# Optimization experiments

Measured on AMD Instinct MI355X. Metric: run time of the kernel, lower is better.

Reference implementation:

```python
import jax, jax.numpy as jnp
import numpy as np

N, E, IN, H, HEADS, L, OUT = 4096, 262144, 64, 128, 4, 2, 2
DH = H // HEADS  # 32, per-head dim for both GAT and global MHA
BN_EPS = 1e-5
NEG_SLOPE = 0.2  # GATConv leaky_relu default


def setup_inputs() -> dict:
    key = jax.random.key(0)
    ks = iter(jax.random.split(key, 32))
    rn = lambda shape, s: jax.random.normal(next(ks), shape, jnp.float32) * s
    return {
        "x": rn((N, IN), 1.0),
        "edge_index": jax.random.randint(next(ks), (2, E), 0, N),
        "w_in": rn((H, IN), IN ** -0.5),
        "b_in": rn((H,), 0.02),
        "w_gat": rn((L, H, H), H ** -0.5),
        "att_src": rn((L, HEADS, DH), 0.1),
        "att_dst": rn((L, HEADS, DH), 0.1),
        "b_gat": rn((L, H), 0.02),
        "w_qkv": rn((L, 3 * H, H), H ** -0.5),
        "b_qkv": rn((L, 3 * H), 0.02),
        "w_o": rn((L, H, H), H ** -0.5),
        "b_o": rn((L, H), 0.02),
        "bn_gamma": 1.0 + rn((L, 3, H), 0.05),
        "bn_beta": rn((L, 3, H), 0.05),
        "w1": rn((L, 2 * H, H), H ** -0.5),
        "b1": rn((L, 2 * H), 0.02),
        "w2": rn((L, H, 2 * H), (2 * H) ** -0.5),
        "b2": rn((L, H), 0.02),
        "w_out": rn((OUT, H), H ** -0.5),
        "b_out": rn((OUT,), 0.02),
    }


def _bn(h, g, b):
    # eval-mode BatchNorm1d with running_mean=0, running_var=1
    return h * (g / jnp.sqrt(1.0 + BN_EPS)) + b


def _gat(x, src, dst, w, a_src, a_dst, bias):
    # GATConv(hidden, hidden//heads, heads=HEADS, add_self_loops=False), concat=True
    xp = (x @ w.T).reshape(N, HEADS, DH)                  # [N, HEADS, DH]
    al_s = jnp.einsum('nhd,hd->nh', xp, a_src)            # [N, HEADS]
    al_d = jnp.einsum('nhd,hd->nh', xp, a_dst)
    logit = al_s[src] + al_d[dst]                         # [E, HEADS]
    logit = jnp.where(logit >= 0, logit, NEG_SLOPE * logit)
    m = jax.ops.segment_max(logit, dst, num_segments=N)   # scatter-softmax over dst
    m = jnp.where(jnp.isfinite(m), m, 0.0)
    e = jnp.exp(logit - m[dst])
    denom = jax.ops.segment_sum(e, dst, num_segments=N)
    alpha = e / (denom[dst] + 1e-16)
    out = jax.ops.segment_sum(alpha[:, :, None] * xp[src], dst, num_segments=N)
    return out.reshape(N, H) + bias


def _mha(x, wqkv, bqkv, wo, bo):
    # torch.nn.MultiheadAttention self-attention over all N nodes (one graph)
    qkv = x @ wqkv.T + bqkv
    q, k, v = jnp.split(qkv, 3, axis=-1)
    q = q.reshape(N, HEADS, DH)
    k = k.reshape(N, HEADS, DH)
    v = v.reshape(N, HEADS, DH)
    scores = jnp.einsum('nhd,mhd->hnm', q, k) / jnp.sqrt(jnp.float32(DH))
    attn = jax.nn.softmax(scores, axis=-1)
    out = jnp.einsum('hnm,mhd->nhd', attn, v).reshape(N, H)
    return out @ wo.T + bo


def reference(x, edge_index, w_in, b_in, w_gat, att_src, att_dst, b_gat,
              w_qkv, b_qkv, w_o, b_o, bn_gamma, bn_beta,
              w1, b1, w2, b2, w_out, b_out):
    src, dst = edge_index[0], edge_index[1]
    h = jax.nn.relu(x @ w_in.T + b_in)
    for l in range(L):
        # GPSConv: local GAT branch (dropout inactive in eval)
        h_loc = _gat(h, src, dst, w_gat[l], att_src[l], att_dst[l], b_gat[l]) + h
        h_loc = _bn(h_loc, bn_gamma[l, 0], bn_beta[l, 0])
        # GPSConv: global attention branch
        h_att = _mha(h, w_qkv[l], b_qkv[l], w_o[l], b_o[l]) + h
        h_att = _bn(h_att, bn_gamma[l, 1], bn_beta[l, 1])
        out = h_loc + h_att
        mlp = jax.nn.relu(out @ w1[l].T + b1[l]) @ w2[l].T + b2[l]
        out = _bn(out + mlp, bn_gamma[l, 2], bn_beta[l, 2])
        # GPSRiskModel residual + relu (dropout inactive in eval)
        h = jax.nn.relu(out + h)
    return h @ w_out.T + b_out
```

## Files before the change

kernel.cpp:

```cpp
#include <hip/hip_runtime.h>

#define NN 4096
#define EE 262144
#define INF_ 64
#define HH 128
#define HEADS 4
#define DH 32
#define LL 2
#define NH (NN * HH)
#define KSPLIT 16
#define L2E 1.4426950408889634f

typedef unsigned short u16;
typedef unsigned int u32;
using bf16x8 = __attribute__((ext_vector_type(8))) short;
using f32x4 = __attribute__((ext_vector_type(4))) float;

__device__ __forceinline__ float bf2f(u16 v) { return __uint_as_float(((u32)v) << 16); }
__device__ __forceinline__ u16 f2bf(float f) {
    u32 u = __float_as_uint(f);
    u32 r = (u + 0x7fffu + ((u >> 16) & 1u)) >> 16;
    return (u16)r;
}
__device__ __forceinline__ u32 encf(float f) {
    u32 b = __float_as_uint(f);
    return (b & 0x80000000u) ? ~b : (b | 0x80000000u);
}
__device__ __forceinline__ float decf(u32 u) {
    u32 b = (u & 0x80000000u) ? (u & 0x7fffffffu) : ~u;
    return __uint_as_float(b);
}

__global__ __launch_bounds__(256) void k_detect(const u16* __restrict__ x, int* __restrict__ flag,
                                                int* __restrict__ cnt, u32* __restrict__ gmax) {
    int t = threadIdx.x;
    for (int i = t; i < NN; i += 256) cnt[i] = 0;
    if (t < 16) gmax[t] = 0;
    __shared__ int cs[256];
    u16 v = x[2 * t];
    int e = (v >> 7) & 0xFF;
    cs[t] = (e >= 100 && e <= 140) ? 1 : 0;
    __syncthreads();
    for (int s = 128; s > 0; s >>= 1) {
        if (t < s) cs[t] += cs[t + s];
        __syncthreads();
    }
    if (t == 0) *flag = (cs[0] >= 128) ? 1 : 0;
}

#define MAXSEG 16
struct SegF { const void* src[MAXSEG]; int dst[MAXSEG]; int n[MAXSEG]; int cnt; };
struct SegB { const void* src[8]; u16* dst[8]; u16* dst2[8]; int n[8]; int cnt; };
__global__ __launch_bounds__(256) void k_prep(SegF SF, float* __restrict__ W, SegB SB,
                                              const int* __restrict__ flag,
                                              const int* __restrict__ dst, int* __restrict__ cnt) {
    int bid = blockIdx.x, t = threadIdx.x;
    if (bid < 96) {
        int seg = bid >> 3, bx = bid & 7;
        if (seg >= SF.cnt) return;
        int n = SF.n[seg];
        float* d = W + SF.dst[seg];
        const void* s = SF.src[seg];
        int f = *flag;
        for (int i = bx * 256 + t; i < n; i += 8 * 256)
            d[i] = f ? bf2f(((const u16*)s)[i]) : ((const float*)s)[i];
    } else if (bid < 992) {
        int b2 = bid - 96;
        int seg = b2 >> 7, bx = b2 & 127;
        if (seg >= SB.cnt) return;
        int f = *flag;
        u16* d = SB.dst[seg];
        u16* d2 = SB.dst2[seg];
        if (f && !d2) return;
        int n = SB.n[seg];
        const void* s = SB.src[seg];
        for (int i = bx * 256 + t; i < n; i += 128 * 256) {
            if (d2) {
                float v = f ? bf2f(((const u16*)s)[i]) : ((const float*)s)[i];
                u16 h = f2bf(v);
                d[i] = h;
                d2[i] = f2bf(v - bf2f(h));
            } else {
                d[i] = f2bf(((const float*)s)[i]);
            }
        }
    } else {
        int e = (bid - 992) * 256 + t;
        if (e < EE) atomicAdd(&cnt[dst[e]], 1);
    }
}

__global__ __launch_bounds__(128) void k_mgemm(const u16* __restrict__ Ahi, const u16* __restrict__ Alo,
                                               const u16* __restrict__ Wc, const u16* __restrict__ Wd,
                                               const int* __restrict__ flag,
                                               const float* __restrict__ bias,
                                               float* __restrict__ outf, u16* __restrict__ outb16,
                                               u16* __restrict__ outhi, u16* __restrict__ outlo,
                                               int K, int J, int relu, int jtiles,
                                               const int* __restrict__ scnt, int* __restrict__ srowstart,
                                               int* __restrict__ scursor) {
    __shared__ int part[128];
    if ((int)blockIdx.y >= jtiles) {
        if (blockIdx.x != 0 || scnt == nullptr) return;
        int t = threadIdx.x;
        int loc[32];
        int s = 0;
#pragma unroll
        for (int i = 0; i < 32; ++i) { loc[i] = s; s += scnt[t * 32 + i]; }
        part[t] = s;
        __syncthreads();
        for (int off = 1; off < 128; off <<= 1) {
            int v = part[t];
            int a = (t >= off) ? part[t - off] : 0;
            __syncthreads();
            part[t] = v + a;
            __syncthreads();
        }
        int base = (t == 0) ? 0 : part[t - 1];
#pragma unroll
        for (int i = 0; i < 32; ++i) {
            srowstart[t * 32 + i] = base + loc[i];
            scursor[t * 32 + i] = base + loc[i];
        }
        return;
    }
    const u16* Wb = (*flag) ? Wd : Wc;
    int wave = threadIdx.x >> 6, lane = threadIdx.x & 63;
    int grp = lane >> 4, lcol = lane & 15;
    int m0 = blockIdx.x * 32 + wave * 16;
    int j0 = blockIdx.y * 64;
    f32x4 acc[4];
#pragma unroll
    for (int s = 0; s < 4; ++s) acc[s] = (f32x4){0.f, 0.f, 0.f, 0.f};
    const u16* ah = Ahi + (size_t)(m0 + lcol) * K + grp * 8;
    const u16* al = Alo + (size_t)(m0 + lcol) * K + grp * 8;
    const u16* wb = Wb + (size_t)(j0 + lcol) * K + grp * 8;
    for (int k = 0; k < K; k += 32) {
        bf16x8 va = *(const bf16x8*)(ah + k);
        bf16x8 vl = *(const bf16x8*)(al + k);
#pragma unroll
        for (int s = 0; s < 4; ++s) {
            bf16x8 vw = *(const bf16x8*)(wb + (size_t)s * 16 * K + k);
            acc[s] = __builtin_amdgcn_mfma_f32_16x16x32_bf16(va, vw, acc[s], 0, 0, 0);
            acc[s] = __builtin_amdgcn_mfma_f32_16x16x32_bf16(vl, vw, acc[s], 0, 0, 0);
        }
    }
#pragma unroll
    for (int s = 0; s < 4; ++s) {
        int col = j0 + s * 16 + lcol;
        float bs = bias ? bias[col] : 0.f;
#pragma unroll
        for (int r = 0; r < 4; ++r) {
            float v = acc[s][r] + bs;
            if (relu) v = fmaxf(v, 0.f);
            size_t idx = (size_t)(m0 + grp * 4 + r) * J + col;
            if (outf) outf[idx] = v;
            if (outb16) outb16[idx] = f2bf(v);
            if (outhi) {
                u16 hv = f2bf(v);
                outhi[idx] = hv;
                outlo[idx] = f2bf(v - bf2f(hv));
            }
        }
    }
}

__global__ __launch_bounds__(128) void k_gemm_gq(const u16* __restrict__ Ahi, const u16* __restrict__ Alo,
                                                 const u16* __restrict__ wgatc, const u16* __restrict__ wgatd,
                                                 const u16* __restrict__ wqkvc, const u16* __restrict__ wqkvd,
                                                 const int* __restrict__ flag,
                                                 const float* __restrict__ bqkv,
                                                 u16* __restrict__ xpb, u16* __restrict__ qkvb,
                                                 const int* __restrict__ esrc_src, const int* __restrict__ esrc_dst,
                                                 int* __restrict__ cursor, int* __restrict__ esrc) {
    if (blockIdx.y >= 8) {
        int b = (blockIdx.y - 8) * 128 + blockIdx.x;
        for (int e = b * 128 + threadIdx.x; e < EE; e += 32768) {
            int d = esrc_dst[e];
            int p = atomicAdd(&cursor[d], 1);
            esrc[p] = esrc_src[e];
        }
        return;
    }
    int wave = threadIdx.x >> 6, lane = threadIdx.x & 63;
    int grp = lane >> 4, lcol = lane & 15;
    int m0 = blockIdx.x * 32 + wave * 16;
    int jb = blockIdx.y;
    int j0 = jb * 64;
    int f = *flag;
    const u16* wgat = f ? wgatd : wgatc;
    const u16* wqkv = f ? wqkvd : wqkvc;
    const u16* Wb = (jb < 2) ? (wgat + (size_t)j0 * HH) : (wqkv + (size_t)(j0 - 128) * HH);
    f32x4 acc[4];
#pragma unroll
    for (int s = 0; s < 4; ++s) acc[s] = (f32x4){0.f, 0.f, 0.f, 0.f};
    const u16* ah = Ahi + (size_t)(m0 + lcol) * HH + grp * 8;
    const u16* al = Alo + (size_t)(m0 + lcol) * HH + grp * 8;
    const u16* wb = Wb + (size_t)lcol * HH + grp * 8;
    for (int k = 0; k < HH; k += 32) {
        bf16x8 va = *(const bf16x8*)(ah + k);
        bf16x8 vl = *(const bf16x8*)(al + k);
#pragma unroll
        for (int s = 0; s < 4; ++s) {
            bf16x8 vw = *(const bf16x8*)(wb + (size_t)s * 16 * HH + k);
            acc[s] = __builtin_amdgcn_mfma_f32_16x16x32_bf16(va, vw, acc[s], 0, 0, 0);
            acc[s] = __builtin_amdgcn_mfma_f32_16x16x32_bf16(vl, vw, acc[s], 0, 0, 0);
        }
    }
    if (jb < 2) {
#pragma unroll
        for (int s = 0; s < 4; ++s) {
            int col = j0 + s * 16 + lcol;
#pragma unroll
            for (int r = 0; r < 4; ++r)
                xpb[(size_t)(m0 + grp * 4 + r) * HH + col] = f2bf(acc[s][r]);
        }
    } else {
#pragma unroll
        for (int s = 0; s < 4; ++s) {
            int colq = j0 - 128 + s * 16 + lcol;
            float bs = bqkv[colq];
#pragma unroll
            for (int r = 0; r < 4; ++r)
                qkvb[(size_t)(m0 + grp * 4 + r) * 384 + colq] = f2bf(acc[s][r] + bs);
        }
    }
}

__global__ __launch_bounds__(256) void k_womlp(const u16* __restrict__ Ahi, const u16* __restrict__ Alo,
                                               const u16* __restrict__ Woc, const u16* __restrict__ Wod,
                                               const u16* __restrict__ W1c, const u16* __restrict__ W1d,
                                               const u16* __restrict__ W2c, const u16* __restrict__ W2d,
                                               const int* __restrict__ flag,
                                               const float* __restrict__ bo, const float* __restrict__ b1,
                                               const float* __restrict__ b2,
                                               const float* __restrict__ gatb, const float* __restrict__ bgat,
                                               const float* __restrict__ gam, const float* __restrict__ bet,
                                               const float* __restrict__ gam2, const float* __restrict__ bet2,
                                               float* __restrict__ hbuf, u16* __restrict__ hhi,
                                               u16* __restrict__ hlo,
                                               const float* __restrict__ wout, const float* __restrict__ bout,
                                               void* __restrict__ yout) {
    __shared__ float Of[16][132];
    __shared__ u16 A2hi[16][136], A2lo[16][136];
    __shared__ u16 Hhi[16][264], Hlo[16][264];
    int f = *flag;
    const u16* Wo = f ? Wod : Woc;
    const u16* W1 = f ? W1d : W1c;
    const u16* W2 = f ? W2d : W2c;
    int wave = threadIdx.x >> 6, lane = threadIdx.x & 63;
    int grp = lane >> 4, lcol = lane & 15;
    int m0 = blockIdx.x * 16;
    float rs = rsqrtf(1.00001f);

    {
        int j0 = wave * 32;
        f32x4 acc[2];
#pragma unroll
        for (int s = 0; s < 2; ++s) acc[s] = (f32x4){0.f, 0.f, 0.f, 0.f};
        const u16* ah = Ahi + (size_t)(m0 + lcol) * HH + grp * 8;
        const u16* al = Alo + (size_t)(m0 + lcol) * HH + grp * 8;
        const u16* wb = Wo + (size_t)(j0 + lcol) * HH + grp * 8;
#pragma unroll
        for (int k = 0; k < HH; k += 32) {
            bf16x8 va = *(const bf16x8*)(ah + k);
            bf16x8 vl = *(const bf16x8*)(al + k);
#pragma unroll
            for (int s = 0; s < 2; ++s) {
                bf16x8 vw = *(const bf16x8*)(wb + (size_t)s * 16 * HH + k);
                acc[s] = __builtin_amdgcn_mfma_f32_16x16x32_bf16(va, vw, acc[s], 0, 0, 0);
                acc[s] = __builtin_amdgcn_mfma_f32_16x16x32_bf16(vl, vw, acc[s], 0, 0, 0);
            }
        }
#pragma unroll
        for (int s = 0; s < 2; ++s) {
            int col = j0 + s * 16 + lcol;
            float bs = bo[col];
            float g0 = gam[col] * rs, b0 = bet[col];
            float g1 = gam[HH + col] * rs, bb1 = bet[HH + col];
            float bg = bgat[col];
#pragma unroll
            for (int r = 0; r < 4; ++r) {
                int row = grp * 4 + r;
                size_t idx = (size_t)(m0 + row) * HH + col;
                float proj = acc[s][r] + bs;
                float hv = hbuf[idx];
                float hl = g0 * (gatb[idx] + bg + hv) + b0;
                float ha = g1 * (proj + hv) + bb1;
                float v = hl + ha;
                Of[row][col] = v;
                u16 hb = f2bf(v);
                A2hi[row][col] = hb;
                A2lo[row][col] = f2bf(v - bf2f(hb));
            }
        }
    }
    __syncthreads();
    {
        int j0 = wave * 64;
        f32x4 acc[4];
#pragma unroll
        for (int s = 0; s < 4; ++s) acc[s] = (f32x4){0.f, 0.f, 0.f, 0.f};
        const u16* wb = W1 + (size_t)(j0 + lcol) * HH + grp * 8;
#pragma unroll
        for (int k = 0; k < HH; k += 32) {
            bf16x8 va = *(const bf16x8*)(&A2hi[lcol][k + grp * 8]);
            bf16x8 vl = *(const bf16x8*)(&A2lo[lcol][k + grp * 8]);
#pragma unroll
            for (int s = 0; s < 4; ++s) {
                bf16x8 vw = *(const bf16x8*)(wb + (size_t)s * 16 * HH + k);
                acc[s] = __builtin_amdgcn_mfma_f32_16x16x32_bf16(va, vw, acc[s], 0, 0, 0);
                acc[s] = __builtin_amdgcn_mfma_f32_16x16x32_bf16(vl, vw, acc[s], 0, 0, 0);
            }
        }
#pragma unroll
        for (int s = 0; s < 4; ++s) {
            int col = j0 + s * 16 + lcol;
            float bs = b1[col];
#pragma unroll
            for (int r = 0; r < 4; ++r) {
                float v = fmaxf(acc[s][r] + bs, 0.f);
                int row = grp * 4 + r;
                u16 hv = f2bf(v);
                Hhi[row][col] = hv;
                Hlo[row][col] = f2bf(v - bf2f(hv));
            }
        }
    }
    __syncthreads();
    {
        int j0 = wave * 32;
        f32x4 acc[2];
#pragma unroll
        for (int s = 0; s < 2; ++s) acc[s] = (f32x4){0.f, 0.f, 0.f, 0.f};
        const u16* wb = W2 + (size_t)(j0 + lcol) * 256 + grp * 8;
#pragma unroll
        for (int k = 0; k < 256; k += 32) {
            bf16x8 va = *(const bf16x8*)(&Hhi[lcol][k + grp * 8]);
            bf16x8 vl = *(const bf16x8*)(&Hlo[lcol][k + grp * 8]);
#pragma unroll
            for (int s = 0; s < 2; ++s) {
                bf16x8 vw = *(const bf16x8*)(wb + (size_t)s * 16 * 256 + k);
                acc[s] = __builtin_amdgcn_mfma_f32_16x16x32_bf16(va, vw, acc[s], 0, 0, 0);
                acc[s] = __builtin_amdgcn_mfma_f32_16x16x32_bf16(vl, vw, acc[s], 0, 0, 0);
            }
        }
#pragma unroll
        for (int s = 0; s < 2; ++s) {
            int col = j0 + s * 16 + lcol;
            float bs = b2[col];
            float g2 = gam2[col] * rs, bb2 = bet2[col];
#pragma unroll
            for (int r = 0; r < 4; ++r) {
                int row = grp * 4 + r;
                size_t idx = (size_t)(m0 + row) * HH + col;
                float mlpo = acc[s][r] + bs;
                float o2 = g2 * (Of[row][col] + mlpo) + bb2;
                float v = fmaxf(o2 + hbuf[idx], 0.f);
                hbuf[idx] = v;
                Of[row][col] = v;
                u16 hb = f2bf(v);
                hhi[idx] = hb;
                hlo[idx] = f2bf(v - bf2f(hb));
            }
        }
    }
    if (yout) {
        __syncthreads();
        int row = threadIdx.x >> 4, sub = threadIdx.x & 15;
        float a0 = 0.f, a1 = 0.f;
#pragma unroll
        for (int k8 = 0; k8 < 8; ++k8) {
            int k = sub * 8 + k8;
            float hv = Of[row][k];
            a0 += hv * wout[k];
            a1 += hv * wout[HH + k];
        }
#pragma unroll
        for (int off = 1; off < 16; off <<= 1) {
            a0 += __shfl_xor(a0, off);
            a1 += __shfl_xor(a1, off);
        }
        if (sub == 0) {
            int n = m0 + row;
            float o0 = a0 + bout[0], o1 = a1 + bout[1];
            if (f) {
                u16* y = (u16*)yout;
                y[n * 2 + 0] = f2bf(o0);
                y[n * 2 + 1] = f2bf(o1);
            } else {
                float* y = (float*)yout;
                y[n * 2 + 0] = o0;
                y[n * 2 + 1] = o1;
            }
        }
    }
}

__global__ __launch_bounds__(256) void k_splitlog(const u16* __restrict__ qkvb,
                                                  float* __restrict__ PM, float* __restrict__ PL,
                                                  u16* __restrict__ PO,
                                                  const u16* __restrict__ xpb,
                                                  const float* __restrict__ asrc,
                                                  const float* __restrict__ adst,
                                                  float* __restrict__ als, float* __restrict__ ald,
                                                  u32* __restrict__ gmax) {
    __shared__ __align__(16) u16 Klds[64][40];
    __shared__ __align__(16) u32 Vlds[32][42];
    __shared__ __align__(16) u16 Plds[4][32][36];

    if (blockIdx.x >= 32 * HEADS * KSPLIT) {
        float* red = (float*)&Klds[0][0];
        int t = (blockIdx.x - 32 * HEADS * KSPLIT) * 256 + threadIdx.x;
        int n = t >> 2, hh = t & 3;
        const u16* xr = xpb + (size_t)n * HH + hh * DH;
        float s1 = 0.f, s2 = 0.f;
#pragma unroll
        for (int d = 0; d < DH; ++d) {
            float v = bf2f(xr[d]);
            s1 += v * asrc[hh * DH + d];
            s2 += v * adst[hh * DH + d];
        }
        als[t] = s1;
        ald[t] = s2;
        int lt = threadIdx.x;
        red[lt] = s1;
        __syncthreads();
        for (int off = 128; off >= 4; off >>= 1) {
            if (lt < off) red[lt] = fmaxf(red[lt], red[lt + off]);
            __syncthreads();
        }
        if (lt < 4) atomicMax(&gmax[lt], encf(red[lt]));
        __syncthreads();
        red[lt] = s2;
        __syncthreads();
        for (int off = 128; off >= 4; off >>= 1) {
            if (lt < off) red[lt] = fmaxf(red[lt], red[lt + off]);
            __syncthreads();
        }
        if (lt < 4) atomicMax(&gmax[4 + lt], encf(red[lt]));
        return;
    }

    const float C1 = 0.17677669529663687f * L2E;
    int head = blockIdx.x & 3;
    int qt = (blockIdx.x >> 2) & 31;
    int ks = blockIdx.x >> 7;
    int tid = threadIdx.x;
    int wave = tid >> 6, lane = tid & 63;
    int grp = lane >> 4, lcol = lane & 15;

    int qrow0 = qt * 128 + wave * 32;
    bf16x8 aQ0 = *(const bf16x8*)(qkvb + (size_t)(qrow0 + lcol) * 384 + head * 32 + grp * 8);
    bf16x8 aQ1 = *(const bf16x8*)(qkvb + (size_t)(qrow0 + 16 + lcol) * 384 + head * 32 + grp * 8);

    short onev = (lcol == 0) ? (short)0x3F80 : (short)0;
    bf16x8 bOne = {onev, onev, onev, onev, onev, onev, onev, onev};

    f32x4 oc00 = {0.f, 0.f, 0.f, 0.f}, oc01 = {0.f, 0.f, 0.f, 0.f};
    f32x4 oc10 = {0.f, 0.f, 0.f, 0.f}, oc11 = {0.f, 0.f, 0.f, 0.f};
    f32x4 ol0 = {0.f, 0.f, 0.f, 0.f}, ol1 = {0.f, 0.f, 0.f, 0.f};
    float msh = -INFINITY;

    int isK = (tid < 128);
    int st = tid & 127;
    int skey = st >> 1, shalf = (st & 1) * 16;
    int vj = st & 15, vc = (st >> 4) & 1, dgrp = st >> 5;
    const u16* kptr = qkvb + 128 + head * 32 + shalf;
    const u16* vptr = qkvb + 256 + head * 32 + dgrp * 8;
    int vk0 = vc * 32 + vj;
    int vk1 = vc * 32 + 16 + vj;

    int kt0 = ks * (NN / KSPLIT);
    bf16x8 r0, r1;
    if (isK) {
        r0 = *(const bf16x8*)(kptr + (size_t)(kt0 + skey) * 384);
        r1 = *(const bf16x8*)(kptr + (size_t)(kt0 + skey) * 384 + 8);
    } else {
        r0 = *(const bf16x8*)(vptr + (size_t)(kt0 + vk0) * 384);
        r1 = *(const bf16x8*)(vptr + (size_t)(kt0 + vk1) * 384);
    }

    const int NT = (NN / KSPLIT) / 64;
    for (int t = 0; t < NT; ++t) {
        if (isK) {
            *(bf16x8*)(&Klds[skey][shalf]) = r0;
            *(bf16x8*)(&Klds[skey][shalf + 8]) = r1;
        } else {
#pragma unroll
            for (int j = 0; j < 8; ++j)
                Vlds[dgrp * 8 + j][vc * 20 + vj] = (u32)(u16)r0[j] | ((u32)(u16)r1[j] << 16);
        }
        __syncthreads();
        if (t + 1 < NT) {
            int kn = kt0 + (t + 1) * 64;
            if (isK) {
                r0 = *(const bf16x8*)(kptr + (size_t)(kn + skey) * 384);
                r1 = *(const bf16x8*)(kptr + (size_t)(kn + skey) * 384 + 8);
            } else {
                r0 = *(const bf16x8*)(vptr + (size_t)(kn + vk0) * 384);
                r1 = *(const bf16x8*)(vptr + (size_t)(kn + vk1) * 384);
            }
        }
        f32x4 sc0[4], sc1[4];
        f32x4 zero = {0.f, 0.f, 0.f, 0.f};
        __builtin_amdgcn_s_setprio(1);
#pragma unroll
        for (int s = 0; s < 4; ++s) {
            bf16x8 bK = *(const bf16x8*)(&Klds[s * 16 + lcol][grp * 8]);
            sc0[s] = __builtin_amdgcn_mfma_f32_16x16x32_bf16(aQ0, bK, zero, 0, 0, 0);
            sc1[s] = __builtin_amdgcn_mfma_f32_16x16x32_bf16(aQ1, bK, zero, 0, 0, 0);
        }
        __builtin_amdgcn_s_setprio(0);
        float mt[8];
#pragma unroll
        for (int s = 0; s < 4; ++s) {
            mt[s] = fmaxf(fmaxf(sc0[s][0], sc0[s][1]), fmaxf(sc0[s][2], sc0[s][3]));
            mt[4 + s] = fmaxf(fmaxf(sc1[s][0], sc1[s][1]), fmaxf(sc1[s][2], sc1[s][3]));
        }
        float mymax = fmaxf(fmaxf(fmaxf(mt[0], mt[1]), fmaxf(mt[2], mt[3])),
                            fmaxf(fmaxf(mt[4], mt[5]), fmaxf(mt[6], mt[7])));
        mymax = fmaxf(mymax, __shfl_xor(mymax, 1));
        mymax = fmaxf(mymax, __shfl_xor(mymax, 2));
        mymax = fmaxf(mymax, __shfl_xor(mymax, 4));
        mymax = fmaxf(mymax, __shfl_xor(mymax, 8));
        float pm = mymax * C1;
        if (__any(pm > msh + 6.0f)) {
            float mnew = fmaxf(msh, pm);
            float cc = __builtin_exp2f(msh - mnew);
            msh = mnew;
            oc00 *= cc; oc01 *= cc; ol0 *= cc;
            oc10 *= cc; oc11 *= cc; ol1 *= cc;
        }
#pragma unroll
        for (int c2 = 0; c2 < 2; ++c2) {
#pragma unroll
            for (int r = 0; r < 4; ++r) {
                float p0 = __builtin_exp2f(__builtin_fmaf(sc0[2 * c2][r], C1, -msh));
                float p1 = __builtin_exp2f(__builtin_fmaf(sc0[2 * c2 + 1][r], C1, -msh));
                *(u32*)(&Plds[wave][grp * 4 + r][2 * lcol]) =
                    __builtin_amdgcn_perm(__float_as_uint(p1), __float_as_uint(p0), 0x07060302u);
                float q0 = __builtin_exp2f(__builtin_fmaf(sc1[2 * c2][r], C1, -msh));
                float q1 = __builtin_exp2f(__builtin_fmaf(sc1[2 * c2 + 1][r], C1, -msh));
                *(u32*)(&Plds[wave][16 + grp * 4 + r][2 * lcol]) =
                    __builtin_amdgcn_perm(__float_as_uint(q1), __float_as_uint(q0), 0x07060302u);
            }
            bf16x8 aP0 = *(const bf16x8*)(&Plds[wave][lcol][grp * 8]);
            bf16x8 aP1 = *(const bf16x8*)(&Plds[wave][16 + lcol][grp * 8]);
            bf16x8 bV0 = *(const bf16x8*)(&Vlds[lcol][c2 * 20 + grp * 4]);
            bf16x8 bV1 = *(const bf16x8*)(&Vlds[16 + lcol][c2 * 20 + grp * 4]);
            __builtin_amdgcn_s_setprio(1);
            oc00 = __builtin_amdgcn_mfma_f32_16x16x32_bf16(aP0, bV0, oc00, 0, 0, 0);
            oc01 = __builtin_amdgcn_mfma_f32_16x16x32_bf16(aP0, bV1, oc01, 0, 0, 0);
            ol0 = __builtin_amdgcn_mfma_f32_16x16x32_bf16(aP0, bOne, ol0, 0, 0, 0);
            oc10 = __builtin_amdgcn_mfma_f32_16x16x32_bf16(aP1, bV0, oc10, 0, 0, 0);
            oc11 = __builtin_amdgcn_mfma_f32_16x16x32_bf16(aP1, bV1, oc11, 0, 0, 0);
            ol1 = __builtin_amdgcn_mfma_f32_16x16x32_bf16(aP1, bOne, ol1, 0, 0, 0);
            __builtin_amdgcn_s_setprio(0);
        }
        __syncthreads();
    }
#pragma unroll
    for (int r = 0; r < 4; ++r) {
        int row0 = qrow0 + grp * 4 + r;
        size_t b0 = ((size_t)row0 * HEADS + head) * KSPLIT + ks;
        PO[b0 * 32 + lcol] = f2bf(oc00[r]);
        PO[b0 * 32 + 16 + lcol] = f2bf(oc01[r]);
        int row1 = row0 + 16;
        size_t b1 = ((size_t)row1 * HEADS + head) * KSPLIT + ks;
        PO[b1 * 32 + lcol] = f2bf(oc10[r]);
        PO[b1 * 32 + 16 + lcol] = f2bf(oc11[r]);
        if (lcol == 0) {
            PM[b0] = msh;
            PL[b0] = ol0[r];
            PM[b1] = msh;
            PL[b1] = ol1[r];
        }
    }
}

#define GCHUNK 256
__global__ __launch_bounds__(128) void k_gatcomb(const int* __restrict__ esrc, const int* __restrict__ rowstart,
                                                 const int* __restrict__ cnt, const float* __restrict__ als,
                                                 const float* __restrict__ ald, const u16* __restrict__ xpb,
                                                 float* __restrict__ gatout, const u32* __restrict__ gmax,
                                                 const float* __restrict__ PM, const float* __restrict__ PL,
                                                 const u16* __restrict__ PO, u16* __restrict__ atthi,
                                                 u16* __restrict__ attlo) {
    __shared__ float red[512];
    __shared__ float elds[GCHUNK * 4];
    __shared__ int slds[GCHUNK];
    int t = threadIdx.x;

    if (blockIdx.x >= NN) {
        int n2 = blockIdx.x - NN;
        float* wn = red;
        if (t < 4 * KSPLIT) {
            int head = t >> 4, ks = t & 15;
            size_t b = ((size_t)n2 * HEADS + head) * KSPLIT + ks;
            float pm = PM[b];
            float m = pm;
#pragma unroll
            for (int off = 1; off < KSPLIT; off <<= 1) m = fmaxf(m, __shfl_xor(m, off));
            float w = __builtin_exp2f(pm - m);
            float lw = PL[b] * w;
#pragma unroll
            for (int off = 1; off < KSPLIT; off <<= 1) lw += __shfl_xor(lw, off);
            wn[t] = w / lw;
        }
        __syncthreads();
        int head = t >> 5, dim = t & 31;
        size_t b0 = ((size_t)n2 * HEADS + head) * KSPLIT;
        float o = 0.f;
#pragma unroll
        for (int k = 0; k < KSPLIT; ++k)
            o += wn[head * KSPLIT + k] * bf2f(PO[(b0 + k) * 32 + dim]);
        size_t idx = (size_t)n2 * HH + t;
        u16 h = f2bf(o);
        atthi[idx] = h;
        attlo[idx] = f2bf(o - bf2f(h));
        return;
    }

    int n = blockIdx.x;
    int base = rowstart[n], c = cnt[n];
    float4 adv = ((const float4*)ald)[n];
    float ad[4] = {adv.x, adv.y, adv.z, adv.w};
    float M2[4];
#pragma unroll
    for (int h = 0; h < 4; ++h) {
        float bound = decf(gmax[h]) + decf(gmax[4 + h]);
        float M = bound >= 0.f ? bound : 0.2f * bound;
        M2[h] = M * L2E;
    }
    float dsum[4] = {0.f, 0.f, 0.f, 0.f};
    int eh = t >> 6, d = t & 63, hd = d >> 4;
    float acc0 = 0.f, acc1 = 0.f;
    int ht = t >> 5;
    for (int ch = 0; ch < c; ch += GCHUNK) {
        int cn = min(GCHUNK, c - ch);
        __syncthreads();
        for (int i = t; i < cn; i += 128) {
            int s = esrc[base + ch + i];
            slds[i] = s;
            float4 as = ((const float4*)als)[s];
            float lg, e;
            lg = as.x + ad[0]; lg = lg >= 0.f ? lg : 0.2f * lg; e = __builtin_exp2f(lg * L2E - M2[0]); elds[i * 4 + 0] = e; dsum[0] += e;
            lg = as.y + ad[1]; lg = lg >= 0.f ? lg : 0.2f * lg; e = __builtin_exp2f(lg * L2E - M2[1]); elds[i * 4 + 1] = e; dsum[1] += e;
            lg = as.z + ad[2]; lg = lg >= 0.f ? lg : 0.2f * lg; e = __builtin_exp2f(lg * L2E - M2[2]); elds[i * 4 + 2] = e; dsum[2] += e;
            lg = as.w + ad[3]; lg = lg >= 0.f ? lg : 0.2f * lg; e = __builtin_exp2f(lg * L2E - M2[3]); elds[i * 4 + 3] = e; dsum[3] += e;
        }
        __syncthreads();
        for (int i = 0; i < cn; i += 4) {
            int i0 = i + eh, i1 = i + 2 + eh;
            int s0 = slds[i0 < cn ? i0 : cn - 1];
            int s1 = slds[i1 < cn ? i1 : cn - 1];
            u32 x0 = *(const u32*)(xpb + (size_t)s0 * HH + 2 * d);
            u32 x1 = *(const u32*)(xpb + (size_t)s1 * HH + 2 * d);
            float w0 = (i0 < cn) ? elds[i0 * 4 + hd] : 0.f;
            float w1 = (i1 < cn) ? elds[i1 * 4 + hd] : 0.f;
            acc0 += w0 * bf2f((u16)(x0 & 0xFFFF)) + w1 * bf2f((u16)(x1 & 0xFFFF));
            acc1 += w0 * bf2f((u16)(x0 >> 16)) + w1 * bf2f((u16)(x1 >> 16));
        }
    }
    __syncthreads();
#pragma unroll
    for (int h = 0; h < 4; ++h) red[h * 128 + t] = dsum[h];
    elds[eh * 128 + 2 * d] = acc0;
    elds[eh * 128 + 2 * d + 1] = acc1;
    __syncthreads();
    for (int s2 = 64; s2 > 0; s2 >>= 1) {
        if (t < s2) {
#pragma unroll
            for (int h = 0; h < 4; ++h)
                red[h * 128 + t] += red[h * 128 + t + s2];
        }
        __syncthreads();
    }
    float accf = elds[t] + elds[128 + t];
    float inv = 1.f / (red[ht * 128] + 1e-16f);
    gatout[(size_t)n * HH + t] = accf * inv;
}

extern "C" void kernel_launch(void* const* d_in, const int* in_sizes, int n_in,
                              void* d_out, int out_size, void* d_ws, size_t ws_size,
                              hipStream_t stream) {
    float* W = (float*)d_ws;
    size_t o = 0;
    auto take = [&](size_t n) { size_t r = o; o += n; return r; };
    size_t pb_in = take(HH);
    size_t pattS = take(LL * HEADS * DH);
    size_t pattD = take(LL * HEADS * DH);
    size_t pb_gat = take(LL * HH);
    size_t pb_qkv = take(LL * 3 * HH);
    size_t pb_o  = take(LL * HH);
    size_t pbn_g = take(LL * 3 * HH);
    size_t pbn_b = take(LL * 3 * HH);
    size_t pb1   = take(LL * 2 * HH);
    size_t pb2   = take(LL * HH);
    size_t pw_out = take(2 * HH);
    size_t pb_out = take(2);
    auto takeb = [&](size_t nu16) { size_t r = o; o += (nu16 + 1) / 2; return r; };
    size_t bw_in  = takeb(HH * INF_);
    size_t bw_gat = takeb(LL * HH * HH);
    size_t bw_qkv = takeb(LL * 3 * HH * HH);
    size_t bw_o   = takeb(LL * HH * HH);
    size_t bw1    = takeb(LL * 2 * HH * HH);
    size_t bw2    = takeb(LL * HH * 2 * HH);
    o = (o + 127) & ~(size_t)127;
    size_t ohbuf = take(NH);
    size_t ogat  = take(NH);
    size_t oals  = take(NN * HEADS);
    size_t oald  = take(NN * HEADS);
    size_t opm   = take(NN * HEADS * KSPLIT);
    size_t opl   = take(NN * HEADS * KSPLIT);
    size_t opo   = takeb((size_t)NN * HEADS * KSPLIT * 32);
    size_t oqkvb = takeb(NN * 384);
    size_t oxpb  = takeb(NH);
    size_t oxhi  = takeb(NN * INF_);
    size_t oxlo  = takeb(NN * INF_);
    size_t ohhi  = takeb(NH);
    size_t ohlo  = takeb(NH);
    size_t oahi  = takeb(NH);
    size_t oalo  = takeb(NH);
    int* ibase    = (int*)(W + o);
    int* iflag    = ibase;
    int* cnt      = ibase + 64;
    int* rowstart = cnt + NN;
    int* cursor   = rowstart + NN;
    int* esrc     = cursor + NN;
    u32* gmax     = (u32*)(esrc + EE);

    float* hbuf = W + ohbuf;
    float* gatb = W + ogat;
    float* als  = W + oals;
    float* ald  = W + oald;
    float* pmb  = W + opm;
    float* plb  = W + opl;
    u16* pob  = (u16*)(W + opo);
    u16* qkvb = (u16*)(W + oqkvb);
    u16* xpb  = (u16*)(W + oxpb);
    u16* xhi = (u16*)(W + oxhi), *xlo = (u16*)(W + oxlo);
    u16* hhi = (u16*)(W + ohhi), *hlo = (u16*)(W + ohlo);
    u16* ahi = (u16*)(W + oahi), *alo = (u16*)(W + oalo);

    const int* src = (const int*)d_in[1];
    const int* dst = (const int*)d_in[1] + EE;
    const u16* dw_in  = (const u16*)d_in[2];
    const u16* dw_gat = (const u16*)d_in[4];
    const u16* dw_qkv = (const u16*)d_in[8];
    const u16* dw_o   = (const u16*)d_in[10];
    const u16* dw1    = (const u16*)d_in[14];
    const u16* dw2    = (const u16*)d_in[16];

    k_detect<<<1, 256, 0, stream>>>((const u16*)d_in[0], iflag, cnt, gmax);

    SegF SF = {};
    int nf = 0;
    auto addf = [&](int idx, size_t off, int n) { SF.src[nf] = d_in[idx]; SF.dst[nf] = (int)off; SF.n[nf] = n; ++nf; };
    addf(3, pb_in, HH);
    addf(5, pattS, LL * HEADS * DH);
    addf(6, pattD, LL * HEADS * DH);
    addf(7, pb_gat, LL * HH);
    addf(9, pb_qkv, LL * 3 * HH);
    addf(11, pb_o, LL * HH);
    addf(12, pbn_g, LL * 3 * HH);
    addf(13, pbn_b, LL * 3 * HH);
    addf(15, pb1, LL * 2 * HH);
    addf(17, pb2, LL * HH);
    addf(18, pw_out, 2 * HH);
    addf(19, pb_out, 2);
    SF.cnt = nf;

    SegB SB = {};
    int nb = 0;
    auto addb = [&](int idx, size_t off, int n, u16* d2) {
        SB.src[nb] = d_in[idx]; SB.dst[nb] = (u16*)(W + off); SB.dst2[nb] = d2; SB.n[nb] = n; ++nb;
    };
    addb(2, bw_in, HH * INF_, nullptr);
    addb(4, bw_gat, LL * HH * HH, nullptr);
    addb(8, bw_qkv, LL * 3 * HH * HH, nullptr);
    addb(10, bw_o, LL * HH * HH, nullptr);
    addb(14, bw1, LL * 2 * HH * HH, nullptr);
    addb(16, bw2, LL * HH * 2 * HH, nullptr);
    SB.src[nb] = d_in[0]; SB.dst[nb] = xhi; SB.dst2[nb] = xlo; SB.n[nb] = NN * INF_; ++nb;
    SB.cnt = nb;

    k_prep<<<2016, 256, 0, stream>>>(SF, W, SB, iflag, dst, cnt);

    k_mgemm<<<dim3(NN / 32, HH / 64 + 1), 128, 0, stream>>>(xhi, xlo, (u16*)(W + bw_in), dw_in, iflag,
                                                            W + pb_in, hbuf, nullptr, hhi, hlo, INF_, HH, 1,
                                                            HH / 64, cnt, rowstart, cursor);

    for (int l = 0; l < LL; ++l) {
        k_gemm_gq<<<dim3(NN / 32, (l == 0) ? 10 : 8), 128, 0, stream>>>(hhi, hlo,
                                                        (u16*)(W + bw_gat) + (size_t)l * HH * HH,
                                                        dw_gat + (size_t)l * HH * HH,
                                                        (u16*)(W + bw_qkv) + (size_t)l * 3 * HH * HH,
                                                        dw_qkv + (size_t)l * 3 * HH * HH,
                                                        iflag, W + pb_qkv + l * 3 * HH, xpb, qkvb,
                                                        src, dst, cursor, esrc);
        k_splitlog<<<32 * HEADS * KSPLIT + (NN * HEADS) / 256, 256, 0, stream>>>(qkvb, pmb, plb, pob, xpb,
                                                                  W + pattS + l * HEADS * DH,
                                                                  W + pattD + l * HEADS * DH,
                                                                  als, ald, gmax + l * 8);
        k_gatcomb<<<2 * NN, 128, 0, stream>>>(esrc, rowstart, cnt, als, ald, xpb, gatb, gmax + l * 8,
                                              pmb, plb, pob, ahi, alo);
        k_womlp<<<NN / 16, 256, 0, stream>>>(ahi, alo,
                                             (u16*)(W + bw_o) + (size_t)l * HH * HH,
                                             dw_o + (size_t)l * HH * HH,
                                             (u16*)(W + bw1) + (size_t)l * 2 * HH * HH,
                                             dw1 + (size_t)l * 2 * HH * HH,
                                             (u16*)(W + bw2) + (size_t)l * HH * 2 * HH,
                                             dw2 + (size_t)l * HH * 2 * HH, iflag,
                                             W + pb_o + l * HH, W + pb1 + l * 2 * HH, W + pb2 + l * HH,
                                             gatb, W + pb_gat + l * HH,
                                             W + pbn_g + l * 3 * HH, W + pbn_b + l * 3 * HH,
                                             W + pbn_g + l * 3 * HH + 2 * HH,
                                             W + pbn_b + l * 3 * HH + 2 * HH,
                                             hbuf, hhi, hlo,
                                             W + pw_out, W + pb_out,
                                             (l == LL - 1) ? d_out : nullptr);
    }
}
```

Measured before the change: 270.5 us.

## Double query rows per wave in split-K attention to reuse K/V tiles

```diff
diff --git a/kernel.cpp b/kernel.cpp
--- a/kernel.cpp
+++ b/kernel.cpp
@@ -397,7 +397,7 @@
     }
 }
 
-__global__ __launch_bounds__(256) void k_splitlog(const u16* __restrict__ qkvb,
+__global__ __launch_bounds__(256, 4) void k_splitlog(const u16* __restrict__ qkvb,
                                                   float* __restrict__ PM, float* __restrict__ PL,
                                                   u16* __restrict__ PO,
                                                   const u16* __restrict__ xpb,
@@ -409,9 +409,9 @@
     __shared__ __align__(16) u32 Vlds[32][42];
     __shared__ __align__(16) u16 Plds[4][32][36];
 
-    if (blockIdx.x >= 32 * HEADS * KSPLIT) {
+    if (blockIdx.x >= 16 * HEADS * KSPLIT) {
         float* red = (float*)&Klds[0][0];
-        int t = (blockIdx.x - 32 * HEADS * KSPLIT) * 256 + threadIdx.x;
+        int t = (blockIdx.x - 16 * HEADS * KSPLIT) * 256 + threadIdx.x;
         int n = t >> 2, hh = t & 3;
         const u16* xr = xpb + (size_t)n * HH + hh * DH;
         float s1 = 0.f, s2 = 0.f;
@@ -444,22 +444,27 @@
 
     const float C1 = 0.17677669529663687f * L2E;
     int head = blockIdx.x & 3;
-    int qt = (blockIdx.x >> 2) & 31;
-    int ks = blockIdx.x >> 7;
+    int qt = (blockIdx.x >> 2) & 15;
+    int ks = blockIdx.x >> 6;
     int tid = threadIdx.x;
     int wave = tid >> 6, lane = tid & 63;
     int grp = lane >> 4, lcol = lane & 15;
 
-    int qrow0 = qt * 128 + wave * 32;
+    int qrow0 = qt * 256 + wave * 64;
     bf16x8 aQ0 = *(const bf16x8*)(qkvb + (size_t)(qrow0 + lcol) * 384 + head * 32 + grp * 8);
     bf16x8 aQ1 = *(const bf16x8*)(qkvb + (size_t)(qrow0 + 16 + lcol) * 384 + head * 32 + grp * 8);
+    bf16x8 aQ2 = *(const bf16x8*)(qkvb + (size_t)(qrow0 + 32 + lcol) * 384 + head * 32 + grp * 8);
+    bf16x8 aQ3 = *(const bf16x8*)(qkvb + (size_t)(qrow0 + 48 + lcol) * 384 + head * 32 + grp * 8);
 
     short onev = (lcol == 0) ? (short)0x3F80 : (short)0;
     bf16x8 bOne = {onev, onev, onev, onev, onev, onev, onev, onev};
 
     f32x4 oc00 = {0.f, 0.f, 0.f, 0.f}, oc01 = {0.f, 0.f, 0.f, 0.f};
     f32x4 oc10 = {0.f, 0.f, 0.f, 0.f}, oc11 = {0.f, 0.f, 0.f, 0.f};
+    f32x4 oc20 = {0.f, 0.f, 0.f, 0.f}, oc21 = {0.f, 0.f, 0.f, 0.f};
+    f32x4 oc30 = {0.f, 0.f, 0.f, 0.f}, oc31 = {0.f, 0.f, 0.f, 0.f};
     f32x4 ol0 = {0.f, 0.f, 0.f, 0.f}, ol1 = {0.f, 0.f, 0.f, 0.f};
+    f32x4 ol2 = {0.f, 0.f, 0.f, 0.f}, ol3 = {0.f, 0.f, 0.f, 0.f};
     float msh = -INFINITY;
 
     int isK = (tid < 128);
@@ -502,61 +507,77 @@
                 r1 = *(const bf16x8*)(vptr + (size_t)(kn + vk1) * 384);
             }
         }
-        f32x4 sc0[4], sc1[4];
-        f32x4 zero = {0.f, 0.f, 0.f, 0.f};
-        __builtin_amdgcn_s_setprio(1);
-#pragma unroll
-        for (int s = 0; s < 4; ++s) {
-            bf16x8 bK = *(const bf16x8*)(&Klds[s * 16 + lcol][grp * 8]);
-            sc0[s] = __builtin_amdgcn_mfma_f32_16x16x32_bf16(aQ0, bK, zero, 0, 0, 0);
-            sc1[s] = __builtin_amdgcn_mfma_f32_16x16x32_bf16(aQ1, bK, zero, 0, 0, 0);
-        }
-        __builtin_amdgcn_s_setprio(0);
-        float mt[8];
-#pragma unroll
-        for (int s = 0; s < 4; ++s) {
-            mt[s] = fmaxf(fmaxf(sc0[s][0], sc0[s][1]), fmaxf(sc0[s][2], sc0[s][3]));
-            mt[4 + s] = fmaxf(fmaxf(sc1[s][0], sc1[s][1]), fmaxf(sc1[s][2], sc1[s][3]));
-        }
-        float mymax = fmaxf(fmaxf(fmaxf(mt[0], mt[1]), fmaxf(mt[2], mt[3])),
-                            fmaxf(fmaxf(mt[4], mt[5]), fmaxf(mt[6], mt[7])));
-        mymax = fmaxf(mymax, __shfl_xor(mymax, 1));
-        mymax = fmaxf(mymax, __shfl_xor(mymax, 2));
-        mymax = fmaxf(mymax, __shfl_xor(mymax, 4));
-        mymax = fmaxf(mymax, __shfl_xor(mymax, 8));
-        float pm = mymax * C1;
-        if (__any(pm > msh + 6.0f)) {
-            float mnew = fmaxf(msh, pm);
-            float cc = __builtin_exp2f(msh - mnew);
-            msh = mnew;
-            oc00 *= cc; oc01 *= cc; ol0 *= cc;
-            oc10 *= cc; oc11 *= cc; ol1 *= cc;
-        }
-#pragma unroll
-        for (int c2 = 0; c2 < 2; ++c2) {
-#pragma unroll
-            for (int r = 0; r < 4; ++r) {
-                float p0 = __builtin_exp2f(__builtin_fmaf(sc0[2 * c2][r], C1, -msh));
-                float p1 = __builtin_exp2f(__builtin_fmaf(sc0[2 * c2 + 1][r], C1, -msh));
-                *(u32*)(&Plds[wave][grp * 4 + r][2 * lcol]) =
-                    __builtin_amdgcn_perm(__float_as_uint(p1), __float_as_uint(p0), 0x07060302u);
-                float q0 = __builtin_exp2f(__builtin_fmaf(sc1[2 * c2][r], C1, -msh));
-                float q1 = __builtin_exp2f(__builtin_fmaf(sc1[2 * c2 + 1][r], C1, -msh));
-                *(u32*)(&Plds[wave][16 + grp * 4 + r][2 * lcol]) =
-                    __builtin_amdgcn_perm(__float_as_uint(q1), __float_as_uint(q0), 0x07060302u);
-            }
-            bf16x8 aP0 = *(const bf16x8*)(&Plds[wave][lcol][grp * 8]);
-            bf16x8 aP1 = *(const bf16x8*)(&Plds[wave][16 + lcol][grp * 8]);
-            bf16x8 bV0 = *(const bf16x8*)(&Vlds[lcol][c2 * 20 + grp * 4]);
-            bf16x8 bV1 = *(const bf16x8*)(&Vlds[16 + lcol][c2 * 20 + grp * 4]);
+#pragma unroll
+        for (int qs = 0; qs < 2; ++qs) {
+            bf16x8 qa = qs ? aQ2 : aQ0;
+            bf16x8 qb = qs ? aQ3 : aQ1;
+            f32x4 sc0[4], sc1[4];
+            f32x4 zero = {0.f, 0.f, 0.f, 0.f};
             __builtin_amdgcn_s_setprio(1);
-            oc00 = __builtin_amdgcn_mfma_f32_16x16x32_bf16(aP0, bV0, oc00, 0, 0, 0);
-            oc01 = __builtin_amdgcn_mfma_f32_16x16x32_bf16(aP0, bV1, oc01, 0, 0, 0);
-            ol0 = __builtin_amdgcn_mfma_f32_16x16x32_bf16(aP0, bOne, ol0, 0, 0, 0);
-            oc10 = __builtin_amdgcn_mfma_f32_16x16x32_bf16(aP1, bV0, oc10, 0, 0, 0);
-            oc11 = __builtin_amdgcn_mfma_f32_16x16x32_bf16(aP1, bV1, oc11, 0, 0, 0);
-            ol1 = __builtin_amdgcn_mfma_f32_16x16x32_bf16(aP1, bOne, ol1, 0, 0, 0);
+#pragma unroll
+            for (int s = 0; s < 4; ++s) {
+                bf16x8 bK = *(const bf16x8*)(&Klds[s * 16 + lcol][grp * 8]);
+                sc0[s] = __builtin_amdgcn_mfma_f32_16x16x32_bf16(qa, bK, zero, 0, 0, 0);
+                sc1[s] = __builtin_amdgcn_mfma_f32_16x16x32_bf16(qb, bK, zero, 0, 0, 0);
+            }
             __builtin_amdgcn_s_setprio(0);
+            float mt[8];
+#pragma unroll
+            for (int s = 0; s < 4; ++s) {
+                mt[s] = fmaxf(fmaxf(sc0[s][0], sc0[s][1]), fmaxf(sc0[s][2], sc0[s][3]));
+                mt[4 + s] = fmaxf(fmaxf(sc1[s][0], sc1[s][1]), fmaxf(sc1[s][2], sc1[s][3]));
+            }
+            float mymax = fmaxf(fmaxf(fmaxf(mt[0], mt[1]), fmaxf(mt[2], mt[3])),
+                                fmaxf(fmaxf(mt[4], mt[5]), fmaxf(mt[6], mt[7])));
+            mymax = fmaxf(mymax, __shfl_xor(mymax, 1));
+            mymax = fmaxf(mymax, __shfl_xor(mymax, 2));
+            mymax = fmaxf(mymax, __shfl_xor(mymax, 4));
+            mymax = fmaxf(mymax, __shfl_xor(mymax, 8));
+            float pm = mymax * C1;
+            if (__any(pm > msh + 6.0f)) {
+                float mnew = fmaxf(msh, pm);
+                float cc = __builtin_exp2f(msh - mnew);
+                msh = mnew;
+                oc00 *= cc; oc01 *= cc; ol0 *= cc;
+                oc10 *= cc; oc11 *= cc; ol1 *= cc;
+                oc20 *= cc; oc21 *= cc; ol2 *= cc;
+                oc30 *= cc; oc31 *= cc; ol3 *= cc;
+            }
+#pragma unroll
+            for (int c2 = 0; c2 < 2; ++c2) {
+#pragma unroll
+                for (int r = 0; r < 4; ++r) {
+                    float p0 = __builtin_exp2f(__builtin_fmaf(sc0[2 * c2][r], C1, -msh));
+                    float p1 = __builtin_exp2f(__builtin_fmaf(sc0[2 * c2 + 1][r], C1, -msh));
+                    *(u32*)(&Plds[wave][grp * 4 + r][2 * lcol]) =
+                        __builtin_amdgcn_perm(__float_as_uint(p1), __float_as_uint(p0), 0x07060302u);
+                    float q0 = __builtin_exp2f(__builtin_fmaf(sc1[2 * c2][r], C1, -msh));
+                    float q1 = __builtin_exp2f(__builtin_fmaf(sc1[2 * c2 + 1][r], C1, -msh));
+                    *(u32*)(&Plds[wave][16 + grp * 4 + r][2 * lcol]) =
+                        __builtin_amdgcn_perm(__float_as_uint(q1), __float_as_uint(q0), 0x07060302u);
+                }
+                bf16x8 aP0 = *(const bf16x8*)(&Plds[wave][lcol][grp * 8]);
+                bf16x8 aP1 = *(const bf16x8*)(&Plds[wave][16 + lcol][grp * 8]);
+                bf16x8 bV0 = *(const bf16x8*)(&Vlds[lcol][c2 * 20 + grp * 4]);
+                bf16x8 bV1 = *(const bf16x8*)(&Vlds[16 + lcol][c2 * 20 + grp * 4]);
+                __builtin_amdgcn_s_setprio(1);
+                if (qs == 0) {
+                    oc00 = __builtin_amdgcn_mfma_f32_16x16x32_bf16(aP0, bV0, oc00, 0, 0, 0);
+                    oc01 = __builtin_amdgcn_mfma_f32_16x16x32_bf16(aP0, bV1, oc01, 0, 0, 0);
+                    ol0 = __builtin_amdgcn_mfma_f32_16x16x32_bf16(aP0, bOne, ol0, 0, 0, 0);
+                    oc10 = __builtin_amdgcn_mfma_f32_16x16x32_bf16(aP1, bV0, oc10, 0, 0, 0);
+                    oc11 = __builtin_amdgcn_mfma_f32_16x16x32_bf16(aP1, bV1, oc11, 0, 0, 0);
+                    ol1 = __builtin_amdgcn_mfma_f32_16x16x32_bf16(aP1, bOne, ol1, 0, 0, 0);
+                } else {
+                    oc20 = __builtin_amdgcn_mfma_f32_16x16x32_bf16(aP0, bV0, oc20, 0, 0, 0);
+                    oc21 = __builtin_amdgcn_mfma_f32_16x16x32_bf16(aP0, bV1, oc21, 0, 0, 0);
+                    ol2 = __builtin_amdgcn_mfma_f32_16x16x32_bf16(aP0, bOne, ol2, 0, 0, 0);
+                    oc30 = __builtin_amdgcn_mfma_f32_16x16x32_bf16(aP1, bV0, oc30, 0, 0, 0);
+                    oc31 = __builtin_amdgcn_mfma_f32_16x16x32_bf16(aP1, bV1, oc31, 0, 0, 0);
+                    ol3 = __builtin_amdgcn_mfma_f32_16x16x32_bf16(aP1, bOne, ol3, 0, 0, 0);
+                }
+                __builtin_amdgcn_s_setprio(0);
+            }
         }
         __syncthreads();
     }
@@ -570,11 +591,19 @@
         size_t b1 = ((size_t)row1 * HEADS + head) * KSPLIT + ks;
         PO[b1 * 32 + lcol] = f2bf(oc10[r]);
         PO[b1 * 32 + 16 + lcol] = f2bf(oc11[r]);
+        int row2 = row0 + 32;
+        size_t b2 = ((size_t)row2 * HEADS + head) * KSPLIT + ks;
+        PO[b2 * 32 + lcol] = f2bf(oc20[r]);
+        PO[b2 * 32 + 16 + lcol] = f2bf(oc21[r]);
+        int row3 = row0 + 48;
+        size_t b3 = ((size_t)row3 * HEADS + head) * KSPLIT + ks;
+        PO[b3 * 32 + lcol] = f2bf(oc30[r]);
+        PO[b3 * 32 + 16 + lcol] = f2bf(oc31[r]);
         if (lcol == 0) {
-            PM[b0] = msh;
-            PL[b0] = ol0[r];
-            PM[b1] = msh;
-            PL[b1] = ol1[r];
+            PM[b0] = msh; PL[b0] = ol0[r];
+            PM[b1] = msh; PL[b1] = ol1[r];
+            PM[b2] = msh; PL[b2] = ol2[r];
+            PM[b3] = msh; PL[b3] = ol3[r];
         }
     }
 }
@@ -800,7 +829,7 @@
                                                         dw_qkv + (size_t)l * 3 * HH * HH,
                                                         iflag, W + pb_qkv + l * 3 * HH, xpb, qkvb,
                                                         src, dst, cursor, esrc);
-        k_splitlog<<<32 * HEADS * KSPLIT + (NN * HEADS) / 256, 256, 0, stream>>>(qkvb, pmb, plb, pob, xpb,
+        k_splitlog<<<16 * HEADS * KSPLIT + (NN * HEADS) / 256, 256, 0, stream>>>(qkvb, pmb, plb, pob, xpb,
                                                                   W + pattS + l * HEADS * DH,
                                                                   W + pattD + l * HEADS * DH,
                                                                   als, ald, gmax + l * 8);
```

After: 273.5 us. About the same (+1.1%).
